# Optimization experiments

Hardware: AMD Instinct MI355X
Metric: run time of the kernel (lower is better)

The kernel has to match this reference:

```python
import jax, jax.numpy as jnp
import numpy as np

NUM_LABELS = 17
MARGIN = 1.0
IGNORE = -100


def setup_inputs() -> dict:
    key = jax.random.key(0)
    k1, k2, k3 = jax.random.split(key, 3)
    B, S, H = 64, 1024, 384
    embeddings = jax.random.normal(k1, (B, S, H), dtype=jnp.float32)
    classifier_w = jax.random.normal(k2, (NUM_LABELS, H), dtype=jnp.float32) * 0.02
    classifier_b = jnp.zeros((NUM_LABELS,), dtype=jnp.float32)
    labels = jax.random.randint(k3, (B, S), 0, NUM_LABELS, dtype=jnp.int64 if jax.config.jax_enable_x64 else jnp.int32)
    attention_mask = jnp.ones((B, S), dtype=jnp.int32)
    return {"embeddings": embeddings, "classifier_w": classifier_w,
            "classifier_b": classifier_b, "labels": labels,
            "attention_mask": attention_mask}


def _total_loss(embeddings, W, b, labels, mask):
    B, S, H = embeddings.shape
    N = B * S
    fe = embeddings.reshape(N, H)          # [N,H] flattened tokens
    fl = labels.reshape(N)
    fm = mask.reshape(N) > 0

    # ----- cross entropy (ignore_index=-100), matches F.cross_entropy mean -----
    logits = fe @ W.T + b                  # [N, L]
    logp = jax.nn.log_softmax(logits, axis=-1)
    safe = jnp.where(fl == IGNORE, 0, fl)
    nll = -jnp.take_along_axis(logp, safe[:, None], axis=1)[:, 0]
    ce_valid = fl != IGNORE
    ce = jnp.sum(jnp.where(ce_valid, nll, 0.0)) / jnp.maximum(jnp.sum(ce_valid), 1)

    # ----- quadruplet loss (deterministic sampling: earliest occurrences) -----
    idx = jnp.arange(N)
    BIG = N  # sentinel index > any real index
    is_ent = fm & (fl > 0)
    non_ent = fm & (fl == 0)
    d_i = jnp.min(jnp.where(non_ent, idx, BIG))   # first non-entity token
    has_non = jnp.any(non_ent)

    def per_type(t):
        m = is_ent & (fl == t)
        order = jnp.sort(jnp.where(m, idx, BIG))
        a_i, p_i = order[0], order[1]             # anchor / positive = first two occurrences
        cnt = jnp.sum(m)
        other = is_ent & (fl != t)
        n_i = jnp.min(jnp.where(other, idx, BIG))  # negative = first other-type entity
        ok = (cnt >= 2) & jnp.any(other) & has_non
        return a_i, p_i, n_i, ok

    types = jnp.arange(1, NUM_LABELS)
    a_i, p_i, n_i, ok = jax.vmap(per_type)(types)  # each [L-1]
    clip = lambda i: jnp.clip(i, 0, N - 1)
    A = fe[clip(a_i)]
    P = fe[clip(p_i)]
    Ng = fe[clip(n_i)]
    D = fe[clip(d_i)][None, :]
    eps = 1e-6  # torch F.pairwise_distance eps added to the difference
    dist = lambda x, y: jnp.sqrt(jnp.sum((x - y + eps) ** 2, axis=-1))
    pd, nd, dd = dist(A, P), dist(A, Ng), dist(A, D)
    ql = jax.nn.relu(pd - nd + MARGIN) + jax.nn.relu(pd - dd + 2.0 * MARGIN)
    qcnt = jnp.sum(ok)
    quad = jnp.sum(jnp.where(ok, ql, 0.0)) / jnp.maximum(qcnt, 1)
    quad = jnp.where(qcnt > 0, quad, 0.0)

    # ----- context loss: adjacent same-entity tokens, mean-per-pair MSE -----
    l0, l1 = labels[:, :-1], labels[:, 1:]
    pair = (l0 != IGNORE) & (l0 == l1) & (l0 > 0)
    mse = jnp.mean((embeddings[:, :-1] - embeddings[:, 1:]) ** 2, axis=-1)  # [B,S-1]
    pc = jnp.sum(pair)
    ctx = jnp.sum(jnp.where(pair, mse, 0.0)) / jnp.maximum(pc, 1)
    ctx = jnp.where(pc > 0, ctx, 0.0)

    return ce + 0.5 * quad + 0.1 * ctx


def reference(embeddings, classifier_w, classifier_b, labels, attention_mask):
    return _total_loss(embeddings, classifier_w, classifier_b, labels, attention_mask)
```

## Files before the change

### kernel.cpp

```cpp
#include <hip/hip_runtime.h>

#define NL 17
#define IGN (-100)
#define HD 384
#define NSEQ 1024
#define NT 65536
#define BIGI NT
#define TPB 256
#define NBLK_MAIN (NT / TPB)
#define NBLK_SCAN 64
#define NCHUNK 12
#define CF4 8

typedef unsigned int u32;
typedef __attribute__((ext_vector_type(8))) short bf16x8;
typedef __attribute__((ext_vector_type(16))) float f32x16;

#define GLOAD_LDS16(g, l) __builtin_amdgcn_global_load_lds(                    \
    (const __attribute__((address_space(1))) u32*)(g),                         \
    (__attribute__((address_space(3))) u32*)(l), 16, 0, 0)

__device__ __forceinline__ u32 cvtpk(float lo, float hi) {
  u32 u;
  asm("v_cvt_pk_bf16_f32 %0, %1, %2" : "=v"(u) : "v"(lo), "v"(hi));
  return u;
}

struct WS {
  float ce_part[NBLK_MAIN];
  float ctx_part[NBLK_MAIN];
  int   ce_cnt[NBLK_MAIN];
  int   ctx_cnt[NBLK_MAIN];
  int   blk_a[NBLK_SCAN][16];
  int   blk_p[NBLK_SCAN][16];
  int   blk_c[NBLK_SCAN][16];
  int   blk_d[NBLK_SCAN];
};

__global__ __launch_bounds__(256) void k_scan(const int* __restrict__ labels,
                                              const int* __restrict__ mask,
                                              WS* __restrict__ ws) {
  __shared__ int comp[1024];
  __shared__ int la[16], lc[16], lp[16], ld;
  const int tid = threadIdx.x, b = blockIdx.x;
  if (tid < 16) { la[tid] = BIGI; lc[tid] = 0; lp[tid] = BIGI; }
  if (tid == 16) ld = BIGI;
  __syncthreads();
  const int base = b * 1024;
#pragma unroll
  for (int k = 0; k < 4; ++k) {
    int l = tid + 256 * k, t = base + l;
    int lb = labels[t];
    int mk = mask[t];
    comp[l] = (mk > 0) ? lb : IGN;
    if (mk > 0) {
      if (lb == 0) atomicMin(&ld, t);
      else if (lb >= 1 && lb < NL) { atomicMin(&la[lb - 1], t); atomicAdd(&lc[lb - 1], 1); }
    }
  }
  __syncthreads();
#pragma unroll
  for (int k = 0; k < 4; ++k) {
    int l = tid + 256 * k, t = base + l;
    int c = comp[l];
    if (c >= 1 && c < NL && t > la[c - 1]) atomicMin(&lp[c - 1], t);
  }
  __syncthreads();
  if (tid < 16) {
    ws->blk_a[b][tid] = la[tid];
    ws->blk_p[b][tid] = lp[tid];
    ws->blk_c[b][tid] = lc[tid];
  }
  if (tid == 16) ws->blk_d[b] = ld;
}

__global__ __launch_bounds__(256, 1) void k_main(const float* __restrict__ emb,
                                                 const float* __restrict__ cw,
                                                 const float* __restrict__ cb,
                                                 const int* __restrict__ labels,
                                                 WS* __restrict__ ws) {
  __shared__ float4 tile[2][TPB * CF4];
  __shared__ float4 sW4[NL * (HD / 4)];
  __shared__ float sce[4], sctx[4];
  __shared__ int   svc[4], spc[4];
  __shared__ float sbctx;
  __shared__ int   sbcnt;

  const int tid = threadIdx.x, lane = tid & 63, wid = tid >> 6;
  const int b = blockIdx.x;
  const int token = b * TPB + tid;

  const float4* cw4 = (const float4*)cw;
  for (int i = tid; i < NL * (HD / 4); i += TPB) {
    int c = i / (HD / 4), q = i % (HD / 4);
    sW4[c * (HD / 4) + (q ^ (c & 7))] = cw4[i];
  }
  __syncthreads();

  const int rb  = tid >> 3;
  const int c4  = tid & 7;
  const int gc4 = c4 ^ (rb & 7);
  const float* src0 = emb + (size_t)b * TPB * HD + (size_t)rb * HD + gc4 * 4;
  const int wbase = __builtin_amdgcn_readfirstlane(wid * 64);

#pragma unroll
  for (int k = 0; k < CF4; ++k)
    GLOAD_LDS16(src0 + (size_t)k * 32 * HD, &tile[0][k * 256 + wbase]);

  const int cls = lane & 31;
  const int kh  = lane >> 5;
  const int clsS = (cls < NL) ? cls : 0;
  const int row0 = wid * 64 + (lane & 31);
  const int row1 = row0 + 32;
  const int r0 = tid;
  const int r1 = (tid < TPB - 1) ? tid + 1 : tid;
  const int x0 = r0 & 7, x1 = r1 & 7;

  f32x16 d0 = {0.f}, d1 = {0.f};
  float ctxacc = 0.f;

  auto bfrag = [&](const float4* tb, int row, int s) -> bf16x8 {
    int g0 = (s * 4 + kh * 2) ^ (row & 7);
    int g1 = (s * 4 + kh * 2 + 1) ^ (row & 7);
    float4 f0 = tb[(row << 3) | g0];
    float4 f1 = tb[(row << 3) | g1];
    union { u32 u[4]; bf16x8 v; } X;
    X.u[0] = cvtpk(f0.x, f0.y); X.u[1] = cvtpk(f0.z, f0.w);
    X.u[2] = cvtpk(f1.x, f1.y); X.u[3] = cvtpk(f1.z, f1.w);
    return X.v;
  };

  auto afrag = [&](int ch, int s) -> bf16x8 {
    union { u32 u[4]; bf16x8 v; } X;
    if (cls < NL) {
      int qa = (ch * 2 + s) * 4 + kh * 2;
      float4 f0 = sW4[clsS * (HD / 4) + ((qa) ^ (cls & 7))];
      float4 f1 = sW4[clsS * (HD / 4) + ((qa + 1) ^ (cls & 7))];
      X.u[0] = cvtpk(f0.x, f0.y); X.u[1] = cvtpk(f0.z, f0.w);
      X.u[2] = cvtpk(f1.x, f1.y); X.u[3] = cvtpk(f1.z, f1.w);
    } else {
      X.u[0] = 0; X.u[1] = 0; X.u[2] = 0; X.u[3] = 0;
    }
    return X.v;
  };

  auto compute = [&](int ch, const float4* tb) {
#pragma unroll
    for (int q = 0; q < CF4; ++q) {
      float4 a  = tb[(r0 << 3) | (q ^ x0)];
      float4 nb = tb[(r1 << 3) | (q ^ x1)];
      float e0 = a.x - nb.x, e1 = a.y - nb.y, e2 = a.z - nb.z, e3 = a.w - nb.w;
      ctxacc = fmaf(e0, e0, fmaf(e1, e1, fmaf(e2, e2, fmaf(e3, e3, ctxacc))));
    }
    bf16x8 a0 = afrag(ch, 0), a1 = afrag(ch, 1);
    bf16x8 b00 = bfrag(tb, row0, 0), b01 = bfrag(tb, row0, 1);
    bf16x8 b10 = bfrag(tb, row1, 0), b11 = bfrag(tb, row1, 1);
    d0 = __builtin_amdgcn_mfma_f32_32x32x16_bf16(a0, b00, d0, 0, 0, 0);
    d0 = __builtin_amdgcn_mfma_f32_32x32x16_bf16(a1, b01, d0, 0, 0, 0);
    d1 = __builtin_amdgcn_mfma_f32_32x32x16_bf16(a0, b10, d1, 0, 0, 0);
    d1 = __builtin_amdgcn_mfma_f32_32x32x16_bf16(a1, b11, d1, 0, 0, 0);
  };

#pragma unroll 1
  for (int ch = 0; ch < NCHUNK - 1; ++ch) {
    const float* srcn = src0 + (size_t)(ch + 1) * 32;
    float4* dstb = tile[(ch + 1) & 1];
#pragma unroll
    for (int k = 0; k < CF4; ++k)
      GLOAD_LDS16(srcn + (size_t)k * 32 * HD, &dstb[k * 256 + wbase]);
    asm volatile("s_waitcnt vmcnt(8)" ::: "memory");
    __builtin_amdgcn_sched_barrier(0);
    __builtin_amdgcn_s_barrier();
    __builtin_amdgcn_sched_barrier(0);
    compute(ch, tile[ch & 1]);
    __builtin_amdgcn_s_barrier();
  }
  asm volatile("s_waitcnt vmcnt(0)" ::: "memory");
  __builtin_amdgcn_sched_barrier(0);
  __builtin_amdgcn_s_barrier();
  __builtin_amdgcn_sched_barrier(0);
  compute(NCHUNK - 1, tile[(NCHUNK - 1) & 1]);
  __syncthreads();

  float* logit = (float*)&tile[0][0];
#pragma unroll
  for (int r = 0; r < 16; ++r) {
    int row = (r & 3) + 8 * (r >> 2) + 4 * kh;
    if (row < NL) {
      logit[(wid * 64 + (lane & 31)) * 21 + row] = d0[r];
      logit[(wid * 64 + 32 + (lane & 31)) * 21 + row] = d1[r];
    }
  }
  __syncthreads();

  float lg[NL];
#pragma unroll
  for (int c = 0; c < NL; ++c) lg[c] = logit[tid * 21 + c] + cb[c];
  float m = lg[0];
#pragma unroll
  for (int c = 1; c < NL; ++c) m = fmaxf(m, lg[c]);
  float s = 0.f;
#pragma unroll
  for (int c = 0; c < NL; ++c) s += __expf(lg[c] - m);
  float lse = m + __logf(s);
  int lb = labels[token];
  int safe = (lb == IGN) ? 0 : lb;
  float ll = 0.f;
#pragma unroll
  for (int c = 0; c < NL; ++c) ll = (c == safe) ? lg[c] : ll;
  bool valid = (lb != IGN);
  float cev = valid ? (lse - ll) : 0.f;

  int nlb = (tid < TPB - 1) ? labels[token + 1] : IGN;
  bool pair = (tid < TPB - 1) && valid && (lb == nlb) && (lb > 0);
  float ctxv = pair ? ctxacc * (1.0f / HD) : 0.f;

  unsigned long long bv = __ballot(valid);
  unsigned long long bp = __ballot(pair);
#pragma unroll
  for (int off = 32; off; off >>= 1) {
    cev  += __shfl_xor(cev, off, 64);
    ctxv += __shfl_xor(ctxv, off, 64);
  }
  if (lane == 0) { sce[wid] = cev; sctx[wid] = ctxv; svc[wid] = __popcll(bv); spc[wid] = __popcll(bp); }

  if (wid == 3) {
    int t = b * TPB + TPB - 1;
    float bc = 0.f; int bn = 0;
    if (((t + 1) & (NSEQ - 1)) != 0) {
      int l0 = labels[t], l1 = labels[t + 1];
      if (l0 != IGN && l0 == l1 && l0 > 0) {
        const float* ra = emb + (size_t)t * HD;
        const float* rbp = ra + HD;
        float a = 0.f;
#pragma unroll
        for (int j = 0; j < 6; ++j) {
          float dd = ra[lane + 64 * j] - rbp[lane + 64 * j];
          a = fmaf(dd, dd, a);
        }
#pragma unroll
        for (int off = 32; off; off >>= 1) a += __shfl_xor(a, off, 64);
        bc = a * (1.0f / HD); bn = 1;
      }
    }
    if (lane == 0) { sbctx = bc; sbcnt = bn; }
  }
  __syncthreads();
  if (tid == 0) {
    ws->ce_part[b]  = sce[0] + sce[1] + sce[2] + sce[3];
    ws->ce_cnt[b]   = svc[0] + svc[1] + svc[2] + svc[3];
    ws->ctx_part[b] = sctx[0] + sctx[1] + sctx[2] + sctx[3] + sbctx;
    ws->ctx_cnt[b]  = spc[0] + spc[1] + spc[2] + spc[3] + sbcnt;
  }
}

__global__ __launch_bounds__(256) void k_final(const float* __restrict__ emb,
                                               WS* __restrict__ ws,
                                               float* __restrict__ out) {
  __shared__ double rce[256], rctx[256];
  __shared__ int rvc[256], rpc[256];
  __shared__ int ga[16], gp[16], gc[16];
  __shared__ int gdsh;
  __shared__ float qs[4]; __shared__ int qc[4];
  const int tid = threadIdx.x, lane = tid & 63, wid = tid >> 6;

  rce[tid]  = ws->ce_part[tid];
  rctx[tid] = ws->ctx_part[tid];
  rvc[tid]  = ws->ce_cnt[tid];
  rpc[tid]  = ws->ctx_cnt[tid];
  __syncthreads();
  for (int s = 128; s > 0; s >>= 1) {
    if (tid < s) {
      rce[tid] += rce[tid + s]; rctx[tid] += rctx[tid + s];
      rvc[tid] += rvc[tid + s]; rpc[tid] += rpc[tid + s];
    }
    __syncthreads();
  }

  if (tid < 16) {
    int m1 = BIGI, m2 = BIGI, cnt = 0;
    for (int bb = 0; bb < NBLK_SCAN; ++bb) {
      int x = ws->blk_a[bb][tid];
      if (x < m1) { m2 = m1; m1 = x; } else if (x < m2) { m2 = x; }
      int y = ws->blk_p[bb][tid];
      if (y < m1) { m2 = m1; m1 = y; } else if (y < m2) { m2 = y; }
      cnt += ws->blk_c[bb][tid];
    }
    ga[tid] = m1; gp[tid] = m2; gc[tid] = cnt;
  }
  if (tid == 16) {
    int d = BIGI;
    for (int bb = 0; bb < NBLK_SCAN; ++bb) d = min(d, ws->blk_d[bb]);
    gdsh = d;
  }
  __syncthreads();

  const int gd = gdsh;
  float qsum = 0.f; int qcnt = 0;
  for (int tt = 0; tt < 4; ++tt) {
    int t = wid * 4 + tt;
    int a = ga[t], p = gp[t], c = gc[t];
    int nmin = BIGI;
#pragma unroll
    for (int u = 0; u < 16; ++u) if (u != t) nmin = min(nmin, ga[u]);
    bool ok = (c >= 2) && (nmin < BIGI) && (gd < BIGI);
    if (ok) {
      const float* A  = emb + (size_t)min(a, NT - 1) * HD;
      const float* P  = emb + (size_t)min(p, NT - 1) * HD;
      const float* Ng = emb + (size_t)min(nmin, NT - 1) * HD;
      const float* D  = emb + (size_t)min(gd, NT - 1) * HD;
      float sap = 0.f, san = 0.f, sad = 0.f;
#pragma unroll
      for (int j = 0; j < 6; ++j) {
        int idx = lane + 64 * j;
        float av = A[idx];
        float d1 = av - P[idx] + 1e-6f;  sap = fmaf(d1, d1, sap);
        float d2 = av - Ng[idx] + 1e-6f; san = fmaf(d2, d2, san);
        float d3 = av - D[idx] + 1e-6f;  sad = fmaf(d3, d3, sad);
      }
#pragma unroll
      for (int off = 32; off; off >>= 1) {
        sap += __shfl_xor(sap, off, 64);
        san += __shfl_xor(san, off, 64);
        sad += __shfl_xor(sad, off, 64);
      }
      float pd = sqrtf(sap), nd = sqrtf(san), dd = sqrtf(sad);
      qsum += fmaxf(pd - nd + 1.0f, 0.f) + fmaxf(pd - dd + 2.0f, 0.f);
      qcnt += 1;
    }
  }
  if (lane == 0) { qs[wid] = qsum; qc[wid] = qcnt; }
  __syncthreads();
  if (tid == 0) {
    double tq = (double)qs[0] + qs[1] + qs[2] + qs[3];
    int tqc = qc[0] + qc[1] + qc[2] + qc[3];
    double ce   = rce[0] / (double)max(rvc[0], 1);
    double ctx  = (rpc[0] > 0) ? rctx[0] / (double)rpc[0] : 0.0;
    double quad = (tqc > 0) ? tq / (double)tqc : 0.0;
    out[0] = (float)(ce + 0.5 * quad + 0.1 * ctx);
  }
}

extern "C" void kernel_launch(void* const* d_in, const int* in_sizes, int n_in,
                              void* d_out, int out_size, void* d_ws, size_t ws_size,
                              hipStream_t stream) {
  const float* emb    = (const float*)d_in[0];
  const float* cw     = (const float*)d_in[1];
  const float* cb     = (const float*)d_in[2];
  const int*   labels = (const int*)d_in[3];
  const int*   mask   = (const int*)d_in[4];
  WS* ws = (WS*)d_ws;
  float* out = (float*)d_out;

  k_scan <<<NBLK_SCAN, 256, 0, stream>>>(labels, mask, ws);
  k_main <<<NBLK_MAIN, 256, 0, stream>>>(emb, cw, cb, labels, ws);
  k_final<<<1, 256, 0, stream>>>(emb, ws, out);
}
```

Baseline: 45.40 us.

## Fuse label scan into main kernel, deepen LDS prefetch, parallelize final merge

Removes the separate k_scan launch by computing per-block first/second occurrence, counts and first non-entity index inside k_main, using LDS atomics over each block's 256 tokens. The embedding tile pipeline goes from double to quad buffering with two chunks in flight, which drops the trailing barrier per iteration. k_final now merges 256 per-block records using a two-level parallel top-2 merge and a tree min. The aim is to save one kernel launch and to hide more load latency, at the cost of more LDS per block (lower occupancy is already fixed at one block) and more per-block records to reduce.

Measured after the change: 36.37 us. 19.9% less time.

```diff
diff --git a/kernel.cpp b/kernel.cpp
--- a/kernel.cpp
+++ b/kernel.cpp
@@ -7,8 +7,7 @@
 #define NT 65536
 #define BIGI NT
 #define TPB 256
-#define NBLK_MAIN (NT / TPB)
-#define NBLK_SCAN 64
+#define NBLK (NT / TPB)
 #define NCHUNK 12
 #define CF4 8
 
@@ -27,64 +26,29 @@
 }
 
 struct WS {
-  float ce_part[NBLK_MAIN];
-  float ctx_part[NBLK_MAIN];
-  int   ce_cnt[NBLK_MAIN];
-  int   ctx_cnt[NBLK_MAIN];
-  int   blk_a[NBLK_SCAN][16];
-  int   blk_p[NBLK_SCAN][16];
-  int   blk_c[NBLK_SCAN][16];
-  int   blk_d[NBLK_SCAN];
+  float ce_part[NBLK];
+  float ctx_part[NBLK];
+  int   ce_cnt[NBLK];
+  int   ctx_cnt[NBLK];
+  int   blk_a[NBLK][16];
+  int   blk_p[NBLK][16];
+  int   blk_c[NBLK][16];
+  int   blk_d[NBLK];
 };
-
-__global__ __launch_bounds__(256) void k_scan(const int* __restrict__ labels,
-                                              const int* __restrict__ mask,
-                                              WS* __restrict__ ws) {
-  __shared__ int comp[1024];
-  __shared__ int la[16], lc[16], lp[16], ld;
-  const int tid = threadIdx.x, b = blockIdx.x;
-  if (tid < 16) { la[tid] = BIGI; lc[tid] = 0; lp[tid] = BIGI; }
-  if (tid == 16) ld = BIGI;
-  __syncthreads();
-  const int base = b * 1024;
-#pragma unroll
-  for (int k = 0; k < 4; ++k) {
-    int l = tid + 256 * k, t = base + l;
-    int lb = labels[t];
-    int mk = mask[t];
-    comp[l] = (mk > 0) ? lb : IGN;
-    if (mk > 0) {
-      if (lb == 0) atomicMin(&ld, t);
-      else if (lb >= 1 && lb < NL) { atomicMin(&la[lb - 1], t); atomicAdd(&lc[lb - 1], 1); }
-    }
-  }
-  __syncthreads();
-#pragma unroll
-  for (int k = 0; k < 4; ++k) {
-    int l = tid + 256 * k, t = base + l;
-    int c = comp[l];
-    if (c >= 1 && c < NL && t > la[c - 1]) atomicMin(&lp[c - 1], t);
-  }
-  __syncthreads();
-  if (tid < 16) {
-    ws->blk_a[b][tid] = la[tid];
-    ws->blk_p[b][tid] = lp[tid];
-    ws->blk_c[b][tid] = lc[tid];
-  }
-  if (tid == 16) ws->blk_d[b] = ld;
-}
 
 __global__ __launch_bounds__(256, 1) void k_main(const float* __restrict__ emb,
                                                  const float* __restrict__ cw,
                                                  const float* __restrict__ cb,
                                                  const int* __restrict__ labels,
+                                                 const int* __restrict__ mask,
                                                  WS* __restrict__ ws) {
-  __shared__ float4 tile[2][TPB * CF4];
+  __shared__ float4 tile[4][TPB * CF4];
   __shared__ float4 sW4[NL * (HD / 4)];
   __shared__ float sce[4], sctx[4];
   __shared__ int   svc[4], spc[4];
   __shared__ float sbctx;
   __shared__ int   sbcnt;
+  __shared__ int   sla[16], slp[16], slc[16], sld;
 
   const int tid = threadIdx.x, lane = tid & 63, wid = tid >> 6;
   const int b = blockIdx.x;
@@ -95,6 +59,8 @@
     int c = i / (HD / 4), q = i % (HD / 4);
     sW4[c * (HD / 4) + (q ^ (c & 7))] = cw4[i];
   }
+  if (tid < 16) { sla[tid] = BIGI; slp[tid] = BIGI; slc[tid] = 0; }
+  if (tid == 16) sld = BIGI;
   __syncthreads();
 
   const int rb  = tid >> 3;
@@ -106,6 +72,9 @@
 #pragma unroll
   for (int k = 0; k < CF4; ++k)
     GLOAD_LDS16(src0 + (size_t)k * 32 * HD, &tile[0][k * 256 + wbase]);
+#pragma unroll
+  for (int k = 0; k < CF4; ++k)
+    GLOAD_LDS16(src0 + 32 + (size_t)k * 32 * HD, &tile[1][k * 256 + wbase]);
 
   const int cls = lane & 31;
   const int kh  = lane >> 5;
@@ -162,24 +131,28 @@
   };
 
 #pragma unroll 1
-  for (int ch = 0; ch < NCHUNK - 1; ++ch) {
-    const float* srcn = src0 + (size_t)(ch + 1) * 32;
-    float4* dstb = tile[(ch + 1) & 1];
+  for (int ch = 0; ch < NCHUNK - 2; ++ch) {
+    const float* srcn = src0 + (size_t)(ch + 2) * 32;
+    float4* dstb = tile[(ch + 2) & 3];
 #pragma unroll
     for (int k = 0; k < CF4; ++k)
       GLOAD_LDS16(srcn + (size_t)k * 32 * HD, &dstb[k * 256 + wbase]);
-    asm volatile("s_waitcnt vmcnt(8)" ::: "memory");
+    asm volatile("s_waitcnt vmcnt(16)" ::: "memory");
     __builtin_amdgcn_sched_barrier(0);
     __builtin_amdgcn_s_barrier();
     __builtin_amdgcn_sched_barrier(0);
-    compute(ch, tile[ch & 1]);
-    __builtin_amdgcn_s_barrier();
-  }
+    compute(ch, tile[ch & 3]);
+  }
+  asm volatile("s_waitcnt vmcnt(8)" ::: "memory");
+  __builtin_amdgcn_sched_barrier(0);
+  __builtin_amdgcn_s_barrier();
+  __builtin_amdgcn_sched_barrier(0);
+  compute(NCHUNK - 2, tile[(NCHUNK - 2) & 3]);
   asm volatile("s_waitcnt vmcnt(0)" ::: "memory");
   __builtin_amdgcn_sched_barrier(0);
   __builtin_amdgcn_s_barrier();
   __builtin_amdgcn_sched_barrier(0);
-  compute(NCHUNK - 1, tile[(NCHUNK - 1) & 1]);
+  compute(NCHUNK - 1, tile[(NCHUNK - 1) & 3]);
   __syncthreads();
 
   float* logit = (float*)&tile[0][0];
@@ -193,6 +166,14 @@
   }
   __syncthreads();
 
+  int lb = labels[token];
+  int mk = mask[token];
+  int lbm = (mk > 0) ? lb : IGN;
+  if (lbm == 0) atomicMin(&sld, token);
+  else if (lbm >= 1 && lbm < NL) { atomicMin(&sla[lbm - 1], token); atomicAdd(&slc[lbm - 1], 1); }
+  __syncthreads();
+  if (lbm >= 1 && lbm < NL && token > sla[lbm - 1]) atomicMin(&slp[lbm - 1], token);
+
   float lg[NL];
 #pragma unroll
   for (int c = 0; c < NL; ++c) lg[c] = logit[tid * 21 + c] + cb[c];
@@ -203,7 +184,6 @@
 #pragma unroll
   for (int c = 0; c < NL; ++c) s += __expf(lg[c] - m);
   float lse = m + __logf(s);
-  int lb = labels[token];
   int safe = (lb == IGN) ? 0 : lb;
   float ll = 0.f;
 #pragma unroll
@@ -246,6 +226,12 @@
     if (lane == 0) { sbctx = bc; sbcnt = bn; }
   }
   __syncthreads();
+  if (tid < 16) {
+    ws->blk_a[b][tid] = sla[tid];
+    ws->blk_p[b][tid] = slp[tid];
+    ws->blk_c[b][tid] = slc[tid];
+  }
+  if (tid == 16) ws->blk_d[b] = sld;
   if (tid == 0) {
     ws->ce_part[b]  = sce[0] + sce[1] + sce[2] + sce[3];
     ws->ce_cnt[b]   = svc[0] + svc[1] + svc[2] + svc[3];
@@ -258,9 +244,9 @@
                                                WS* __restrict__ ws,
                                                float* __restrict__ out) {
   __shared__ double rce[256], rctx[256];
-  __shared__ int rvc[256], rpc[256];
+  __shared__ int rvc[256], rpc[256], rd[256];
+  __shared__ int M1[256], M2[256], CN[256];
   __shared__ int ga[16], gp[16], gc[16];
-  __shared__ int gdsh;
   __shared__ float qs[4]; __shared__ int qc[4];
   const int tid = threadIdx.x, lane = tid & 63, wid = tid >> 6;
 
@@ -268,34 +254,45 @@
   rctx[tid] = ws->ctx_part[tid];
   rvc[tid]  = ws->ce_cnt[tid];
   rpc[tid]  = ws->ctx_cnt[tid];
+  rd[tid]   = ws->blk_d[tid];
+
+  {
+    const int type = tid & 15, seg = tid >> 4;
+    int m1 = BIGI, m2 = BIGI, cnt = 0;
+#pragma unroll 4
+    for (int k = 0; k < 16; ++k) {
+      int bb = seg * 16 + k;
+      int x = ws->blk_a[bb][type];
+      if (x < m1) { m2 = m1; m1 = x; } else if (x < m2) { m2 = x; }
+      int y = ws->blk_p[bb][type];
+      if (y < m1) { m2 = m1; m1 = y; } else if (y < m2) { m2 = y; }
+      cnt += ws->blk_c[bb][type];
+    }
+    M1[tid] = m1; M2[tid] = m2; CN[tid] = cnt;
+  }
   __syncthreads();
   for (int s = 128; s > 0; s >>= 1) {
     if (tid < s) {
       rce[tid] += rce[tid + s]; rctx[tid] += rctx[tid + s];
       rvc[tid] += rvc[tid + s]; rpc[tid] += rpc[tid + s];
+      rd[tid] = min(rd[tid], rd[tid + s]);
     }
     __syncthreads();
   }
-
   if (tid < 16) {
     int m1 = BIGI, m2 = BIGI, cnt = 0;
-    for (int bb = 0; bb < NBLK_SCAN; ++bb) {
-      int x = ws->blk_a[bb][tid];
-      if (x < m1) { m2 = m1; m1 = x; } else if (x < m2) { m2 = x; }
-      int y = ws->blk_p[bb][tid];
-      if (y < m1) { m2 = m1; m1 = y; } else if (y < m2) { m2 = y; }
-      cnt += ws->blk_c[bb][tid];
+    for (int seg = 0; seg < 16; ++seg) {
+      int a1 = M1[seg * 16 + tid], a2 = M2[seg * 16 + tid];
+      int n1 = min(m1, a1);
+      int n2 = min(max(m1, a1), min(m2, a2));
+      m1 = n1; m2 = n2;
+      cnt += CN[seg * 16 + tid];
     }
     ga[tid] = m1; gp[tid] = m2; gc[tid] = cnt;
   }
-  if (tid == 16) {
-    int d = BIGI;
-    for (int bb = 0; bb < NBLK_SCAN; ++bb) d = min(d, ws->blk_d[bb]);
-    gdsh = d;
-  }
-  __syncthreads();
-
-  const int gd = gdsh;
+  __syncthreads();
+
+  const int gd = rd[0];
   float qsum = 0.f; int qcnt = 0;
   for (int tt = 0; tt < 4; ++tt) {
     int t = wid * 4 + tt;
@@ -352,7 +349,6 @@
   WS* ws = (WS*)d_ws;
   float* out = (float*)d_out;
 
-  k_scan <<<NBLK_SCAN, 256, 0, stream>>>(labels, mask, ws);
-  k_main <<<NBLK_MAIN, 256, 0, stream>>>(emb, cw, cb, labels, ws);
+  k_main <<<NBLK, 256, 0, stream>>>(emb, cw, cb, labels, mask, ws);
   k_final<<<1, 256, 0, stream>>>(emb, ws, out);
 }
```
